# Performance work log

Measured on AMD Instinct MI355X. Metric: run time of the kernel, lower is better.

The kernel has to match this reference:

```python
import jax, jax.numpy as jnp
import numpy as np

N = 32768      # total points (8 clouds x 4096)
B = 8          # clouds in batch
D_IN = 64      # input feature dim
M = 8192       # sampled centers (ratio=0.25)
K = 32         # knn neighbors
R = 0.2        # ball radius
DIMS = [D_IN + 3, 128, 128, 256]  # edge MLP (PointNetConv local_nn)


def setup_inputs() -> dict:
    key = jax.random.key(0)
    ks = jax.random.split(key, 10)
    x = jax.random.normal(ks[0], (N, D_IN), jnp.float32)
    pos = jax.random.uniform(ks[1], (N, 3), jnp.float32)  # unit cube
    batch = jnp.repeat(jnp.arange(B, dtype=jnp.int32), N // B)
    # deterministic stand-in for torch.sort(torch.randperm(N)[:M])
    idx = jnp.sort(jax.random.permutation(ks[2], N)[:M]).astype(jnp.int32)
    params = {}
    for i in range(3):
        fan_in = DIMS[i]
        params[f"W{i+1}"] = jax.random.normal(ks[3 + 2 * i], (DIMS[i], DIMS[i + 1]), jnp.float32) / np.sqrt(fan_in)
        params[f"b{i+1}"] = jnp.zeros((DIMS[i + 1],), jnp.float32)
    return {"x": x, "pos": pos, "batch": batch, "idx": idx, **params}


def _knn_ball(pos, batch, idx, k, r):
    """Batched KNN restricted to same cloud, then radius mask (ball query)."""
    centers = pos[idx]                                   # [M, 3]
    d2 = (jnp.sum(centers ** 2, -1)[:, None]
          + jnp.sum(pos ** 2, -1)[None, :]
          - 2.0 * centers @ pos.T)                       # [M, N]
    same = batch[idx][:, None] == batch[None, :]
    d2 = jnp.where(same, d2, jnp.inf)
    neg_d2, nbr = jax.lax.top_k(-d2, k)                  # [M, K]
    valid = (-neg_d2) <= r * r                           # ball-query radius clip
    return nbr, valid


def reference(x, pos, batch, idx, W1, b1, W2, b2, W3, b3):
    nbr, valid = _knn_ball(pos, batch, idx, K, R)        # [M,K], [M,K]
    centers = pos[idx]                                   # [M, 3]
    rel = pos[nbr] - centers[:, None, :]                 # [M, K, 3]
    feat = jnp.concatenate([x[nbr], rel], axis=-1)       # [M, K, D_IN+3]
    h = jax.nn.relu(feat @ W1 + b1)
    h = jax.nn.relu(h @ W2 + b2)
    h = jax.nn.relu(h @ W3 + b3)                         # [M, K, 256]
    # max aggregation over valid neighbors (scatter-max equivalent)
    h = jnp.where(valid[:, :, None], h, -jnp.inf)
    out = jnp.max(h, axis=1)                             # [M, 256]
    return out, pos[idx], batch[idx]
```

## Files before the change

kernel.cpp:

```cpp
#include <hip/hip_runtime.h>


typedef unsigned short u16;
typedef unsigned int u32;
typedef unsigned long long u64;
typedef __bf16 bf16x8 __attribute__((ext_vector_type(8)));
typedef float floatx4 __attribute__((ext_vector_type(4)));

#define PCLOUD 4096
#define DIN    64
#define MCENT  8192
#define KNBR   32
#define CAP    448

#define OFF_LIST  0
#define OFF_HIST  14336
#define OFF_NBRL  14848
#define OFF_CNT   15360
#define OFF_CEN   15392
#define OFF_BCL   15456

__device__ inline u16 f2bf(float f) {
    u32 b = __float_as_uint(f);
    b += 0x7fffu + ((b >> 16) & 1u);
    return (u16)(b >> 16);
}
__device__ inline u32 cvtpk(float a, float b) {
    u32 r;
    asm("v_cvt_pk_bf16_f32 %0, %1, %2" : "=v"(r) : "v"(a), "v"(b));
    return r;
}
__device__ inline u64 wave_min_u64(u64 v) {
    #pragma unroll
    for (int off = 32; off; off >>= 1) {
        u64 o = __shfl_xor((unsigned long long)v, off);
        if (o < v) v = o;
    }
    return v;
}
__device__ inline u64 d2key(float d2, int j) {
    u32 u = __float_as_uint(d2);
    u = (u & 0x80000000u) ? ~u : (u | 0x80000000u);
    return ((u64)u << 32) | (u32)j;
}
__device__ inline int key_bucket(u64 k) {
    u32 hi = (u32)(k >> 32);
    if (hi < 0x80000000u) return 0;
    float d2 = __uint_as_float(hi & 0x7fffffffu);
    float t = d2 * 25.0f;
    float b = 32.0f * t * __builtin_sqrtf(t);
    int bi = (int)b;
    return bi > 31 ? 31 : (bi < 0 ? 0 : bi);
}

__global__ void prep_kernel(const float* __restrict__ W1, const float* __restrict__ W2,
                            const float* __restrict__ W3, uint4* __restrict__ ws) {
    int t = blockIdx.x * 256 + threadIdx.x;
    int g = t >> 11, r = t & 2047;
    int n = r >> 4, kc = r & 15;
    const float* W; int rs, n0, krows;
    if (g == 0)      { W = W1; rs = 128; n0 = 0;   krows = 67;  }
    else if (g == 1) { W = W2; rs = 128; n0 = 0;   krows = 128; }
    else if (g == 2) { W = W3; rs = 256; n0 = 0;   krows = 128; }
    else             { W = W3; rs = 256; n0 = 128; krows = 128; }
    u16 e[8];
    #pragma unroll
    for (int j = 0; j < 8; j++) {
        int k = kc * 8 + j;
        e[j] = (k < krows) ? f2bf(W[(size_t)k * rs + n0 + n]) : (u16)0;
    }
    ws[(g << 11) + (n << 4) + (kc ^ (n & 7))] = *(const uint4*)e;
}

__device__ __forceinline__ uint4 ldB_ws(const uint4* __restrict__ ws4, int blk, int cb, int m16) {
    return ws4[blk * 256 + (m16 << 4) + (cb ^ (m16 & 7))];
}
__device__ __forceinline__ uint4 ldB_fb(const float* __restrict__ W, int rs, int col,
                                        int cb, int krows) {
    u16 e[8];
    #pragma unroll
    for (int j = 0; j < 8; j++) {
        int k = cb * 8 + j;
        e[j] = (k < krows) ? f2bf(W[(size_t)k * rs + col]) : (u16)0;
    }
    return *(const uint4*)e;
}

__device__ __forceinline__ void push_hit(int c, float d2, int j,
                                         int* acnt, u64* lists) {
    int p = atomicAdd(&acnt[c], 1);
    if (p < CAP) lists[c * CAP + p] = d2key(d2, j);
}

template <bool WS>
__global__ __launch_bounds__(256, 4) void sa_kernel(
    const float* __restrict__ x, const float* __restrict__ pos,
    const int* __restrict__ batch, const int* __restrict__ idx,
    const float* __restrict__ W1, const float* __restrict__ b1,
    const float* __restrict__ W2, const float* __restrict__ b2,
    const float* __restrict__ W3, const float* __restrict__ b3,
    const uint4* __restrict__ ws4, float* __restrict__ out) {
    __shared__ __align__(16) char smem[32768];
    u64*  lists = (u64*)(smem + OFF_LIST);
    u32*  hist  = (u32*)(smem + OFF_HIST);
    int*  nbrl  = (int*)(smem + OFF_NBRL);
    int*  acnt  = (int*)(smem + OFF_CNT);
    int*  cnt2  = (int*)(smem + OFF_CNT + 16);
    float4* cen = (float4*)(smem + OFF_CEN);
    int*  bcls  = (int*)(smem + OFF_BCL);
    uint4* sA4  = (uint4*)smem;

    int tid = threadIdx.x, w = tid >> 6, l = tid & 63;
    int bid = blockIdx.x;
    int m0 = ((bid & 7) << 10) + ((bid >> 3) << 2);
    int m = m0 + w;
    int ic = idx[m] & (8 * PCLOUD - 1);
    float cx = pos[ic * 3], cy = pos[ic * 3 + 1], cz = pos[ic * 3 + 2];
    float sc = __fadd_rn(__fadd_rn(__fmul_rn(cx, cx), __fmul_rn(cy, cy)), __fmul_rn(cz, cz));
    int bcl = batch[ic] & 7;
    int base = bcl << 12;
    const float R2 = 0.04f;

    if (l == 0) { cen[w] = make_float4(cx, cy, cz, sc); bcls[w] = bcl; }
    if (tid < 4) { acnt[tid] = 0; cnt2[tid] = 0; }
    if (l == 1) {
        float* o1 = out + MCENT * 256;
        o1[m * 3] = cx; o1[m * 3 + 1] = cy; o1[m * 3 + 2] = cz;
        (o1 + MCENT * 3)[m] = (float)bcl;
    }
    __syncthreads();

    bool uni = (bcls[0] == bcls[1]) && (bcls[1] == bcls[2]) && (bcls[2] == bcls[3]);
    if (uni) {
        float4 cA = cen[0], cB = cen[1], cC = cen[2], cD = cen[3];
        float nAx = -2.0f * cA.x, nAy = -2.0f * cA.y, nAz = -2.0f * cA.z;
        float nBx = -2.0f * cB.x, nBy = -2.0f * cB.y, nBz = -2.0f * cB.z;
        float nCx = -2.0f * cC.x, nCy = -2.0f * cC.y, nCz = -2.0f * cC.z;
        float nDx = -2.0f * cD.x, nDy = -2.0f * cD.y, nDz = -2.0f * cD.z;
        int jb = bcls[0] << 12;
        const float4* pb4 = (const float4*)(pos + (size_t)jb * 3);

#define TEST1(NX, NY, NZ, SW, CI, SP, PX, PY, PZ, J) { \
    float d2 = __builtin_fmaf((NX), (PX), __builtin_fmaf((NY), (PY), \
               __builtin_fmaf((NZ), (PZ), (SW) + (SP)))); \
    if (d2 <= R2) push_hit(CI, d2, J, acnt, lists); }
#define TESTP(PX, PY, PZ, J) { \
    float sp = __builtin_fmaf((PX), (PX), __builtin_fmaf((PY), (PY), (PZ) * (PZ))); \
    TEST1(nAx, nAy, nAz, cA.w, 0, sp, PX, PY, PZ, J) \
    TEST1(nBx, nBy, nBz, cB.w, 1, sp, PX, PY, PZ, J) \
    TEST1(nCx, nCy, nCz, cC.w, 2, sp, PX, PY, PZ, J) \
    TEST1(nDx, nDy, nDz, cD.w, 3, sp, PX, PY, PZ, J) }

        #pragma unroll
        for (int it = 0; it < 4; it++) {
            int tq = it * 256 + tid;
            float4 q0 = pb4[tq * 3], q1 = pb4[tq * 3 + 1], q2 = pb4[tq * 3 + 2];
            int j0 = jb + tq * 4;
            TESTP(q0.x, q0.y, q0.z, j0)
            TESTP(q0.w, q1.x, q1.y, j0 + 1)
            TESTP(q1.z, q1.w, q2.x, j0 + 2)
            TESTP(q2.y, q2.z, q2.w, j0 + 3)
        }
#undef TESTP
#undef TEST1
    } else {
        float nx = -2.0f * cx, ny = -2.0f * cy, nz = -2.0f * cz;
        for (int t = l; t < PCLOUD; t += 64) {
            int j = base + t;
            float px = pos[j * 3], py = pos[j * 3 + 1], pz = pos[j * 3 + 2];
            float sp = __builtin_fmaf(px, px, __builtin_fmaf(py, py, pz * pz));
            float d2 = __builtin_fmaf(nx, px, __builtin_fmaf(ny, py,
                       __builtin_fmaf(nz, pz, sc + sp)));
            if (d2 <= R2) push_hit(w, d2, j, acnt, lists);
        }
    }
    __syncthreads();

    int c = acnt[w];
    int nsel = c < KNBR ? c : KNBR;
    u64* mylist = lists + w * CAP;

    int selj = -1;
    if (c <= KNBR) {
        if (l < c) selj = (int)(u32)mylist[l];
    } else if (c <= CAP) {
        u64 kk[7];
        int bk[7];
        if (l < 32) hist[w * 32 + l] = 0;
        #pragma unroll
        for (int i = 0; i < 7; i++) kk[i] = (l + i * 64 < c) ? mylist[l + i * 64] : ~0ull;
        #pragma unroll
        for (int i = 0; i < 7; i++) {
            bk[i] = 32;
            if (kk[i] != ~0ull) {
                bk[i] = key_bucket(kk[i]);
                atomicAdd(&hist[w * 32 + bk[i]], 1u);
            }
        }
        int hv = (l < 32) ? (int)hist[w * 32 + l] : 0;
        #pragma unroll
        for (int off = 1; off <= 16; off <<= 1) {
            int o = __shfl_up(hv, off);
            if (l >= off) hv += o;
        }
        u64 ge = __ballot((l < 32) && (hv >= KNBR));
        int B = __ffsll((unsigned long long)ge) - 1;
        int S = (B == 0) ? 0 : __shfl(hv, B - 1);
        #pragma unroll
        for (int i = 0; i < 7; i++) {
            if (kk[i] != ~0ull) {
                if (bk[i] < B) { int p = atomicAdd(&cnt2[w], 1); nbrl[w * 32 + p] = (int)(u32)kk[i]; }
                if (bk[i] != B) kk[i] = ~0ull;
            }
        }
        int need = KNBR - S;
        u64 last = 0;
        for (int r = 0; r < need; r++) {
            u64 mn = ~0ull;
            #pragma unroll
            for (int i = 0; i < 7; i++) if (kk[i] > last && kk[i] < mn) mn = kk[i];
            mn = wave_min_u64(mn);
            if (l == 0) nbrl[w * 32 + S + r] = (int)(u32)mn;
            last = mn;
        }
        if (l < KNBR) selj = nbrl[w * 32 + l];
    } else {
        float nx = -2.0f * cx, ny = -2.0f * cy, nz = -2.0f * cz;
        u64 last = 0;
        for (int r = 0; r < KNBR; r++) {
            u64 mn = ~0ull;
            for (int t = l; t < PCLOUD; t += 64) {
                int j = base + t;
                float px = pos[j * 3], py = pos[j * 3 + 1], pz = pos[j * 3 + 2];
                float sp = __builtin_fmaf(px, px, __builtin_fmaf(py, py, pz * pz));
                float d2 = __builtin_fmaf(nx, px, __builtin_fmaf(ny, py,
                           __builtin_fmaf(nz, pz, sc + sp)));
                if (d2 <= R2) { u64 kf = d2key(d2, j); if (kf > last && kf < mn) mn = kf; }
            }
            mn = wave_min_u64(mn);
            if (l == r) selj = (int)(u32)mn;
            last = mn;
        }
    }
    __syncthreads();

    {
        int h = l & 1, rl = l >> 1;
        int row = w * 32 + rl;
        int j = __shfl(selj, rl);
        int xv = row & 7;
        uint4* dst = sA4 + row * 16;
        uint4 z; z.x = z.y = z.z = z.w = 0;
        if (j >= 0) {
            const float4* sx = (const float4*)(x + (size_t)j * DIN);
            if (h == 0) {
                float4 f[12];
                #pragma unroll
                for (int i = 0; i < 12; i++) f[i] = sx[i];
                #pragma unroll
                for (int c0 = 0; c0 < 6; c0++) {
                    uint4 pv;
                    pv.x = cvtpk(f[c0 * 2].x, f[c0 * 2].y);
                    pv.y = cvtpk(f[c0 * 2].z, f[c0 * 2].w);
                    pv.z = cvtpk(f[c0 * 2 + 1].x, f[c0 * 2 + 1].y);
                    pv.w = cvtpk(f[c0 * 2 + 1].z, f[c0 * 2 + 1].w);
                    dst[c0 ^ xv] = pv;
                }
            } else {
                float4 f[4];
                #pragma unroll
                for (int i = 0; i < 4; i++) f[i] = sx[12 + i];
                float rx = pos[j * 3] - cx, ry = pos[j * 3 + 1] - cy, rz = pos[j * 3 + 2] - cz;
                #pragma unroll
                for (int c0 = 0; c0 < 2; c0++) {
                    uint4 pv;
                    pv.x = cvtpk(f[c0 * 2].x, f[c0 * 2].y);
                    pv.y = cvtpk(f[c0 * 2].z, f[c0 * 2].w);
                    pv.z = cvtpk(f[c0 * 2 + 1].x, f[c0 * 2 + 1].y);
                    pv.w = cvtpk(f[c0 * 2 + 1].z, f[c0 * 2 + 1].w);
                    dst[(6 + c0) ^ xv] = pv;
                }
                uint4 rc; rc.x = cvtpk(rx, ry); rc.y = cvtpk(rz, 0.0f); rc.z = 0; rc.w = 0;
                dst[8 ^ xv] = rc;
                dst[9 ^ xv] = z; dst[10 ^ xv] = z; dst[11 ^ xv] = z;
            }
        } else {
            if (h == 0) {
                #pragma unroll
                for (int c0 = 0; c0 < 6; c0++) dst[c0 ^ xv] = z;
            } else {
                #pragma unroll
                for (int c0 = 6; c0 < 12; c0++) dst[c0 ^ xv] = z;
            }
        }
    }

    int m16 = l & 15, quad = l >> 4;
    int r0 = w * 32;
    const floatx4 vzero = {0.f, 0.f, 0.f, 0.f};

#define LDB(BLK, CB, W, RS, COL, KR) \
    (WS ? ldB_ws(ws4, (BLK), (CB), m16) : ldB_fb((W), (RS), (COL), (CB), (KR)))

#define EPI12(BPTR, S, ACC) { \
    float4 bb = ((const float4*)(BPTR))[(S) * 4 + quad]; \
    _Pragma("unroll") \
    for (int t = 0; t < 2; t++) { \
        int rr = r0 + t * 16 + m16; \
        uint2 pv; \
        pv.x = cvtpk(fmaxf(ACC[t][0] + bb.x, 0.f), fmaxf(ACC[t][1] + bb.y, 0.f)); \
        pv.y = cvtpk(fmaxf(ACC[t][2] + bb.z, 0.f), fmaxf(ACC[t][3] + bb.w, 0.f)); \
        *(uint2*)(smem + rr * 256 + ((((S) * 2 + (quad >> 1)) ^ (rr & 7)) << 4) + ((quad & 1) << 3)) = pv; \
    } }

    {
        bf16x8 a1[3][2];
        #pragma unroll
        for (int ki = 0; ki < 3; ki++)
            #pragma unroll
            for (int t = 0; t < 2; t++) {
                int row = r0 + t * 16 + m16;
                a1[ki][t] = __builtin_bit_cast(bf16x8, sA4[row * 16 + ((ki * 4 + quad) ^ (row & 7))]);
            }
        uint4 p0[3], p1[3];
        #pragma unroll
        for (int ki = 0; ki < 3; ki++) p0[ki] = LDB(0, ki * 4 + quad, W1, 128, m16, 67);
        #pragma unroll
        for (int ki = 0; ki < 3; ki++) p1[ki] = LDB(1, ki * 4 + quad, W1, 128, 16 + m16, 67);
        #pragma unroll
        for (int s = 0; s < 8; s += 2) {
            {
                floatx4 acc[2] = {vzero, vzero};
                __builtin_amdgcn_s_setprio(1);
                #pragma unroll
                for (int ki = 0; ki < 3; ki++) {
                    bf16x8 b = __builtin_bit_cast(bf16x8, p0[ki]);
                    #pragma unroll
                    for (int t = 0; t < 2; t++)
                        acc[t] = __builtin_amdgcn_mfma_f32_16x16x32_bf16(b, a1[ki][t], acc[t], 0, 0, 0);
                }
                __builtin_amdgcn_s_setprio(0);
                if (s + 2 < 8) {
                    #pragma unroll
                    for (int ki = 0; ki < 3; ki++)
                        p0[ki] = LDB(s + 2, ki * 4 + quad, W1, 128, (s + 2) * 16 + m16, 67);
                }
                EPI12(b1, s, acc);
            }
            {
                floatx4 acc[2] = {vzero, vzero};
                __builtin_amdgcn_s_setprio(1);
                #pragma unroll
                for (int ki = 0; ki < 3; ki++) {
                    bf16x8 b = __builtin_bit_cast(bf16x8, p1[ki]);
                    #pragma unroll
                    for (int t = 0; t < 2; t++)
                        acc[t] = __builtin_amdgcn_mfma_f32_16x16x32_bf16(b, a1[ki][t], acc[t], 0, 0, 0);
                }
                __builtin_amdgcn_s_setprio(0);
                if (s + 3 < 8) {
                    #pragma unroll
                    for (int ki = 0; ki < 3; ki++)
                        p1[ki] = LDB(s + 3, ki * 4 + quad, W1, 128, (s + 3) * 16 + m16, 67);
                }
                EPI12(b1, s + 1, acc);
            }
        }
    }

    {
        bf16x8 a2[4][2];
        #pragma unroll
        for (int ki = 0; ki < 4; ki++)
            #pragma unroll
            for (int t = 0; t < 2; t++) {
                int row = r0 + t * 16 + m16;
                a2[ki][t] = __builtin_bit_cast(bf16x8, sA4[row * 16 + ((ki * 4 + quad) ^ (row & 7))]);
            }
        uint4 p0[4], p1[4];
        #pragma unroll
        for (int ki = 0; ki < 4; ki++) p0[ki] = LDB(8, ki * 4 + quad, W2, 128, m16, 128);
        #pragma unroll
        for (int ki = 0; ki < 4; ki++) p1[ki] = LDB(9, ki * 4 + quad, W2, 128, 16 + m16, 128);
        #pragma unroll
        for (int s = 0; s < 8; s += 2) {
            {
                floatx4 acc[2] = {vzero, vzero};
                __builtin_amdgcn_s_setprio(1);
                #pragma unroll
                for (int ki = 0; ki < 4; ki++) {
                    bf16x8 b = __builtin_bit_cast(bf16x8, p0[ki]);
                    #pragma unroll
                    for (int t = 0; t < 2; t++)
                        acc[t] = __builtin_amdgcn_mfma_f32_16x16x32_bf16(b, a2[ki][t], acc[t], 0, 0, 0);
                }
                __builtin_amdgcn_s_setprio(0);
                if (s + 2 < 8) {
                    #pragma unroll
                    for (int ki = 0; ki < 4; ki++)
                        p0[ki] = LDB(8 + s + 2, ki * 4 + quad, W2, 128, (s + 2) * 16 + m16, 128);
                }
                EPI12(b2, s, acc);
            }
            {
                floatx4 acc[2] = {vzero, vzero};
                __builtin_amdgcn_s_setprio(1);
                #pragma unroll
                for (int ki = 0; ki < 4; ki++) {
                    bf16x8 b = __builtin_bit_cast(bf16x8, p1[ki]);
                    #pragma unroll
                    for (int t = 0; t < 2; t++)
                        acc[t] = __builtin_amdgcn_mfma_f32_16x16x32_bf16(b, a2[ki][t], acc[t], 0, 0, 0);
                }
                __builtin_amdgcn_s_setprio(0);
                if (s + 3 < 8) {
                    #pragma unroll
                    for (int ki = 0; ki < 4; ki++)
                        p1[ki] = LDB(8 + s + 3, ki * 4 + quad, W2, 128, (s + 3) * 16 + m16, 128);
                }
                EPI12(b2, s + 1, acc);
            }
        }
    }

#define EPI3(S, ACC) { \
    int col = (S) * 16 + m16; \
    float bias = b3[col]; \
    float mv = 0.0f; \
    _Pragma("unroll") \
    for (int t = 0; t < 2; t++) \
        _Pragma("unroll") \
        for (int i = 0; i < 4; i++) { \
            int k = t * 16 + quad * 4 + i; \
            float v = fmaxf(ACC[t][i] + bias, 0.0f); \
            if (k < nsel) mv = fmaxf(mv, v); \
        } \
    mv = fmaxf(mv, __shfl_xor(mv, 16)); \
    mv = fmaxf(mv, __shfl_xor(mv, 32)); \
    if (quad == 0) out[(m0 + w) * 256 + col] = mv; }

    {
        bf16x8 a3[4][2];
        #pragma unroll
        for (int ki = 0; ki < 4; ki++)
            #pragma unroll
            for (int t = 0; t < 2; t++) {
                int row = r0 + t * 16 + m16;
                a3[ki][t] = __builtin_bit_cast(bf16x8, sA4[row * 16 + ((ki * 4 + quad) ^ (row & 7))]);
            }
        uint4 p0[4], p1[4];
        #pragma unroll
        for (int ki = 0; ki < 4; ki++) p0[ki] = LDB(16, ki * 4 + quad, W3, 256, m16, 128);
        #pragma unroll
        for (int ki = 0; ki < 4; ki++) p1[ki] = LDB(17, ki * 4 + quad, W3, 256, 16 + m16, 128);
        #pragma unroll
        for (int s = 0; s < 16; s += 2) {
            {
                floatx4 acc[2] = {vzero, vzero};
                __builtin_amdgcn_s_setprio(1);
                #pragma unroll
                for (int ki = 0; ki < 4; ki++) {
                    bf16x8 b = __builtin_bit_cast(bf16x8, p0[ki]);
                    #pragma unroll
                    for (int t = 0; t < 2; t++)
                        acc[t] = __builtin_amdgcn_mfma_f32_16x16x32_bf16(a3[ki][t], b, acc[t], 0, 0, 0);
                }
                __builtin_amdgcn_s_setprio(0);
                if (s + 2 < 16) {
                    #pragma unroll
                    for (int ki = 0; ki < 4; ki++)
                        p0[ki] = LDB(16 + s + 2, ki * 4 + quad, W3, 256, (s + 2) * 16 + m16, 128);
                }
                EPI3(s, acc);
            }
            {
                floatx4 acc[2] = {vzero, vzero};
                __builtin_amdgcn_s_setprio(1);
                #pragma unroll
                for (int ki = 0; ki < 4; ki++) {
                    bf16x8 b = __builtin_bit_cast(bf16x8, p1[ki]);
                    #pragma unroll
                    for (int t = 0; t < 2; t++)
                        acc[t] = __builtin_amdgcn_mfma_f32_16x16x32_bf16(a3[ki][t], b, acc[t], 0, 0, 0);
                }
                __builtin_amdgcn_s_setprio(0);
                if (s + 3 < 16) {
                    #pragma unroll
                    for (int ki = 0; ki < 4; ki++)
                        p1[ki] = LDB(16 + s + 3, ki * 4 + quad, W3, 256, (s + 3) * 16 + m16, 128);
                }
                EPI3(s + 1, acc);
            }
        }
    }
#undef LDB
#undef EPI12
#undef EPI3
}

extern "C" void kernel_launch(void* const* d_in, const int* in_sizes, int n_in,
                              void* d_out, int out_size, void* d_ws, size_t ws_size,
                              hipStream_t stream) {
    const float* x     = (const float*)d_in[0];
    const float* pos   = (const float*)d_in[1];
    const int*   batch = (const int*)d_in[2];
    const int*   idx   = (const int*)d_in[3];
    const float* W1    = (const float*)d_in[4];
    const float* b1    = (const float*)d_in[5];
    const float* W2    = (const float*)d_in[6];
    const float* b2    = (const float*)d_in[7];
    const float* W3    = (const float*)d_in[8];
    const float* b3    = (const float*)d_in[9];
    float* out = (float*)d_out;
    uint4* ws4 = (uint4*)d_ws;

    if (ws_size >= 131072) {
        hipLaunchKernelGGL(prep_kernel, dim3(32), dim3(256), 0, stream, W1, W2, W3, ws4);
        hipLaunchKernelGGL((sa_kernel<true>), dim3(MCENT / 4), dim3(256), 0, stream,
                           x, pos, batch, idx, W1, b1, W2, b2, W3, b3, ws4, out);
    } else {
        hipLaunchKernelGGL((sa_kernel<false>), dim3(MCENT / 4), dim3(256), 0, stream,
                           x, pos, batch, idx, W1, b1, W2, b2, W3, b3, ws4, out);
    }
}
```

Measured before the change: 161.2 us.

## Process eight centers per block to share each cloud's position scan

Doubles the block from 4 to 8 waves, one center per wave, and doubles the shared-memory layout to hold eight candidate lists. Each point loaded during the ball-query scan is now tested against all eight centers, which halves the global position reads and scan loop iterations per center. The per-wave center tests are generalised into a loop over WAVES. In exchange each block uses 64KB of LDS and 512 threads, which can lower the number of resident blocks and waves per CU, and more centers now compete for the shared hit-counter atomics.

```diff
diff --git a/kernel.cpp b/kernel.cpp
--- a/kernel.cpp
+++ b/kernel.cpp
@@ -12,13 +12,14 @@
 #define MCENT  8192
 #define KNBR   32
 #define CAP    448
+#define WAVES  8
 
 #define OFF_LIST  0
-#define OFF_HIST  14336
-#define OFF_NBRL  14848
-#define OFF_CNT   15360
-#define OFF_CEN   15392
-#define OFF_BCL   15456
+#define OFF_HIST  28672
+#define OFF_NBRL  29696
+#define OFF_CNT   30720
+#define OFF_CEN   30784
+#define OFF_BCL   30912
 
 __device__ inline u16 f2bf(float f) {
     u32 b = __float_as_uint(f);
@@ -93,26 +94,26 @@
 }
 
 template <bool WS>
-__global__ __launch_bounds__(256, 4) void sa_kernel(
+__global__ __launch_bounds__(512, 4) void sa_kernel(
     const float* __restrict__ x, const float* __restrict__ pos,
     const int* __restrict__ batch, const int* __restrict__ idx,
     const float* __restrict__ W1, const float* __restrict__ b1,
     const float* __restrict__ W2, const float* __restrict__ b2,
     const float* __restrict__ W3, const float* __restrict__ b3,
     const uint4* __restrict__ ws4, float* __restrict__ out) {
-    __shared__ __align__(16) char smem[32768];
+    __shared__ __align__(16) char smem[65536];
     u64*  lists = (u64*)(smem + OFF_LIST);
     u32*  hist  = (u32*)(smem + OFF_HIST);
     int*  nbrl  = (int*)(smem + OFF_NBRL);
     int*  acnt  = (int*)(smem + OFF_CNT);
-    int*  cnt2  = (int*)(smem + OFF_CNT + 16);
+    int*  cnt2  = (int*)(smem + OFF_CNT + 32);
     float4* cen = (float4*)(smem + OFF_CEN);
     int*  bcls  = (int*)(smem + OFF_BCL);
     uint4* sA4  = (uint4*)smem;
 
     int tid = threadIdx.x, w = tid >> 6, l = tid & 63;
     int bid = blockIdx.x;
-    int m0 = ((bid & 7) << 10) + ((bid >> 3) << 2);
+    int m0 = ((bid & 7) << 10) + ((bid >> 3) << 3);
     int m = m0 + w;
     int ic = idx[m] & (8 * PCLOUD - 1);
     float cx = pos[ic * 3], cy = pos[ic * 3 + 1], cz = pos[ic * 3 + 2];
@@ -122,7 +123,7 @@
     const float R2 = 0.04f;
 
     if (l == 0) { cen[w] = make_float4(cx, cy, cz, sc); bcls[w] = bcl; }
-    if (tid < 4) { acnt[tid] = 0; cnt2[tid] = 0; }
+    if (tid < WAVES) { acnt[tid] = 0; cnt2[tid] = 0; }
     if (l == 1) {
         float* o1 = out + MCENT * 256;
         o1[m * 3] = cx; o1[m * 3 + 1] = cy; o1[m * 3 + 2] = cz;
@@ -130,30 +131,32 @@
     }
     __syncthreads();
 
-    bool uni = (bcls[0] == bcls[1]) && (bcls[1] == bcls[2]) && (bcls[2] == bcls[3]);
+    bool uni = true;
+    #pragma unroll
+    for (int cc = 1; cc < WAVES; cc++) uni = uni && (bcls[cc] == bcls[0]);
     if (uni) {
-        float4 cA = cen[0], cB = cen[1], cC = cen[2], cD = cen[3];
-        float nAx = -2.0f * cA.x, nAy = -2.0f * cA.y, nAz = -2.0f * cA.z;
-        float nBx = -2.0f * cB.x, nBy = -2.0f * cB.y, nBz = -2.0f * cB.z;
-        float nCx = -2.0f * cC.x, nCy = -2.0f * cC.y, nCz = -2.0f * cC.z;
-        float nDx = -2.0f * cD.x, nDy = -2.0f * cD.y, nDz = -2.0f * cD.z;
+        float4 cw[WAVES];
+        float nx[WAVES], ny[WAVES], nz[WAVES];
+        #pragma unroll
+        for (int cc = 0; cc < WAVES; cc++) {
+            cw[cc] = cen[cc];
+            nx[cc] = -2.0f * cw[cc].x; ny[cc] = -2.0f * cw[cc].y; nz[cc] = -2.0f * cw[cc].z;
+        }
         int jb = bcls[0] << 12;
         const float4* pb4 = (const float4*)(pos + (size_t)jb * 3);
 
-#define TEST1(NX, NY, NZ, SW, CI, SP, PX, PY, PZ, J) { \
-    float d2 = __builtin_fmaf((NX), (PX), __builtin_fmaf((NY), (PY), \
-               __builtin_fmaf((NZ), (PZ), (SW) + (SP)))); \
-    if (d2 <= R2) push_hit(CI, d2, J, acnt, lists); }
 #define TESTP(PX, PY, PZ, J) { \
     float sp = __builtin_fmaf((PX), (PX), __builtin_fmaf((PY), (PY), (PZ) * (PZ))); \
-    TEST1(nAx, nAy, nAz, cA.w, 0, sp, PX, PY, PZ, J) \
-    TEST1(nBx, nBy, nBz, cB.w, 1, sp, PX, PY, PZ, J) \
-    TEST1(nCx, nCy, nCz, cC.w, 2, sp, PX, PY, PZ, J) \
-    TEST1(nDx, nDy, nDz, cD.w, 3, sp, PX, PY, PZ, J) }
-
-        #pragma unroll
-        for (int it = 0; it < 4; it++) {
-            int tq = it * 256 + tid;
+    _Pragma("unroll") \
+    for (int cc = 0; cc < WAVES; cc++) { \
+        float d2 = __builtin_fmaf(nx[cc], (PX), __builtin_fmaf(ny[cc], (PY), \
+                   __builtin_fmaf(nz[cc], (PZ), cw[cc].w + sp))); \
+        if (d2 <= R2) push_hit(cc, d2, (J), acnt, lists); \
+    } }
+
+        #pragma unroll
+        for (int it = 0; it < 2; it++) {
+            int tq = it * 512 + tid;
             float4 q0 = pb4[tq * 3], q1 = pb4[tq * 3 + 1], q2 = pb4[tq * 3 + 2];
             int j0 = jb + tq * 4;
             TESTP(q0.x, q0.y, q0.z, j0)
@@ -162,7 +165,6 @@
             TESTP(q2.y, q2.z, q2.w, j0 + 3)
         }
 #undef TESTP
-#undef TEST1
     } else {
         float nx = -2.0f * cx, ny = -2.0f * cy, nz = -2.0f * cz;
         for (int t = l; t < PCLOUD; t += 64) {
@@ -516,10 +518,10 @@
 
     if (ws_size >= 131072) {
         hipLaunchKernelGGL(prep_kernel, dim3(32), dim3(256), 0, stream, W1, W2, W3, ws4);
-        hipLaunchKernelGGL((sa_kernel<true>), dim3(MCENT / 4), dim3(256), 0, stream,
+        hipLaunchKernelGGL((sa_kernel<true>), dim3(MCENT / WAVES), dim3(512), 0, stream,
                            x, pos, batch, idx, W1, b1, W2, b2, W3, b3, ws4, out);
     } else {
-        hipLaunchKernelGGL((sa_kernel<false>), dim3(MCENT / 4), dim3(256), 0, stream,
+        hipLaunchKernelGGL((sa_kernel<false>), dim3(MCENT / WAVES), dim3(512), 0, stream,
                            x, pos, batch, idx, W1, b1, W2, b2, W3, b3, ws4, out);
     }
 }
```

Result: slower. 164.8 us (+2.2%).
